# Kernel tuning notes

Hardware: AMD Instinct MI355X
Metric: run time of the kernel (lower is better)

Reference implementation:

```python
import jax, jax.numpy as jnp
import numpy as np

D = 768
NH = 12
HD = D // NH
N_MLP = 3072
LN_EPS = 1e-6


def layer_norm(x, g, b, eps=LN_EPS):
    mu = jnp.mean(x, axis=-1, keepdims=True)
    var = jnp.mean(jnp.square(x - mu), axis=-1, keepdims=True)
    return (x - mu) * jax.lax.rsqrt(var + eps) * g + b


def setup_inputs() -> dict:
    key = jax.random.key(0)
    ks = jax.random.split(key, 6)
    x = jax.random.normal(ks[0], (2, 4096, D), dtype=jnp.float32)
    # torch Linear weights are (out, in); init std=0.02, zero bias
    W_qkv = 0.02 * jax.random.normal(ks[1], (3 * D, D), dtype=jnp.float32)
    b_qkv = jnp.zeros((3 * D,), dtype=jnp.float32)
    W_proj = 0.02 * jax.random.normal(ks[2], (D, D), dtype=jnp.float32)
    b_proj = jnp.zeros((D,), dtype=jnp.float32)
    W1 = 0.02 * jax.random.normal(ks[3], (N_MLP, D), dtype=jnp.float32)
    b1 = jnp.zeros((N_MLP,), dtype=jnp.float32)
    W2 = 0.02 * jax.random.normal(ks[4], (D, N_MLP), dtype=jnp.float32)
    b2 = jnp.zeros((D,), dtype=jnp.float32)
    g1 = jnp.ones((D,), dtype=jnp.float32)
    beta1 = jnp.zeros((D,), dtype=jnp.float32)
    g2 = jnp.ones((D,), dtype=jnp.float32)
    beta2 = jnp.zeros((D,), dtype=jnp.float32)
    return dict(x=x, W_qkv=W_qkv, b_qkv=b_qkv, W_proj=W_proj, b_proj=b_proj,
                W1=W1, b1=b1, W2=W2, b2=b2,
                g1=g1, beta1=beta1, g2=g2, beta2=beta2)


def reference(x, W_qkv, b_qkv, W_proj, b_proj, W1, b1, W2, b2, g1, beta1, g2, beta2):
    B, T, d = x.shape
    scale = HD ** (-0.5)
    # --- attention branch (pre-norm) ---
    h = layer_norm(x, g1, beta1)
    qkv = h @ W_qkv.T + b_qkv                      # [B,T,3d]
    qkv = qkv.reshape(B, T, 3, NH, HD)
    q, k, v = qkv[:, :, 0], qkv[:, :, 1], qkv[:, :, 2]  # [B,T,NH,HD]
    logits = jnp.einsum('bthc,bshc->bhts', q, k) * scale
    attn = jax.nn.softmax(logits, axis=-1)
    out = jnp.einsum('bhts,bshc->bthc', attn, v).reshape(B, T, d)
    out = out @ W_proj.T + b_proj
    x = x + out
    # --- MLP branch (pre-norm) ---
    h = layer_norm(x, g2, beta2)
    h = jax.nn.gelu(h @ W1.T + b1, approximate=False)
    h = h @ W2.T + b2
    return x + h
```

## Files before the change

kernel.cpp:

```cpp
#include <hip/hip_runtime.h>
#include <cmath>

typedef __attribute__((ext_vector_type(4))) float f32x4;
typedef __attribute__((ext_vector_type(16))) float f32x16;
typedef __attribute__((ext_vector_type(8))) __bf16 bf16x8;
typedef __attribute__((ext_vector_type(8))) unsigned short u16x8;
typedef __attribute__((ext_vector_type(4))) unsigned short u16x4;
typedef __attribute__((ext_vector_type(2))) unsigned int u32x2;
typedef __attribute__((ext_vector_type(4))) unsigned int u32x4;

#define DEV __device__ __forceinline__

DEV unsigned short f2b(float v) {
  __bf16 b = (__bf16)v;
  return __builtin_bit_cast(unsigned short, b);
}

DEV unsigned int cvtpk(float lo, float hi) {
  unsigned int r;
  asm("v_cvt_pk_bf16_f32 %0, %1, %2" : "=v"(r) : "v"(lo), "v"(hi));
  return r;
}

DEV float exp2a(float x) {
  float r;
  asm("v_exp_f32 %0, %1" : "=v"(r) : "v"(x));
  return r;
}

DEV void swap32(unsigned int& x, unsigned int& y) {
  asm("v_permlane32_swap_b32 %0, %1" : "+v"(x), "+v"(y));
}

DEV u32x2 tr_b16(const unsigned short* p) {
  u32x2 r;
  asm volatile("ds_read_b64_tr_b16 %0, %1"
               : "=v"(r)
               : "v"((unsigned int)(unsigned long long)p)
               : "memory");
  return r;
}

DEV void gll16(const void* g, const void* l) {
  __builtin_amdgcn_global_load_lds(
      (const __attribute__((address_space(1))) unsigned int*)(unsigned long long)g,
      (__attribute__((address_space(3))) unsigned int*)(unsigned int)(unsigned long long)l,
      16, 0, 0);
}

__global__ void k_cvt_bf16(const float* __restrict__ src,
                           unsigned short* __restrict__ dst, int n4) {
  int i = blockIdx.x * blockDim.x + threadIdx.x;
  if (i >= n4) return;
  float4 v = ((const float4*)src)[i];
  u16x4 o = {f2b(v.x), f2b(v.y), f2b(v.z), f2b(v.w)};
  *(u16x4*)(dst + (size_t)i * 4) = o;
}

__global__ void k_ln(const float* __restrict__ x, const float* __restrict__ g,
                     const float* __restrict__ be, unsigned short* __restrict__ out) {
  int row = blockIdx.x;
  int l = threadIdx.x;
  const float* xr = x + (size_t)row * 768;
  float4 v[3];
  float s = 0.f, sq = 0.f;
#pragma unroll
  for (int j = 0; j < 3; ++j) {
    v[j] = ((const float4*)xr)[l + 64 * j];
    s += v[j].x + v[j].y + v[j].z + v[j].w;
    sq += v[j].x * v[j].x + v[j].y * v[j].y + v[j].z * v[j].z + v[j].w * v[j].w;
  }
#pragma unroll
  for (int m = 1; m < 64; m <<= 1) {
    s += __shfl_xor(s, m);
    sq += __shfl_xor(sq, m);
  }
  float mu = s * (1.f / 768.f);
  float var = sq * (1.f / 768.f) - mu * mu;
  float rs = rsqrtf(var + 1e-6f);
  unsigned short* orow = out + (size_t)row * 768;
#pragma unroll
  for (int j = 0; j < 3; ++j) {
    int c4 = l + 64 * j;
    float4 gv = ((const float4*)g)[c4];
    float4 bv = ((const float4*)be)[c4];
    u16x4 o = {f2b((v[j].x - mu) * rs * gv.x + bv.x),
               f2b((v[j].y - mu) * rs * gv.y + bv.y),
               f2b((v[j].z - mu) * rs * gv.z + bv.z),
               f2b((v[j].w - mu) * rs * gv.w + bv.w)};
    *(u16x4*)(orow + c4 * 4) = o;
  }
}

template <int MODE>
__global__ __launch_bounds__(256) void k_gemm(
    const unsigned short* __restrict__ A, const unsigned short* __restrict__ Bw,
    const float* __restrict__ bias, const float* __restrict__ res,
    void* __restrict__ outp, int N, int K) {
  __shared__ unsigned short As[128 * 32];
  __shared__ unsigned short Bs[128 * 32];
  const int tid = threadIdx.x;
  const int w = tid >> 6, l = tid & 63;
  const int wr = w >> 1, wc = w & 1;
  const int lr = l & 15, lg = l >> 4;
  const int nwg = gridDim.x * gridDim.y;
  const int bid = blockIdx.y * gridDim.x + blockIdx.x;
  const int swz = (bid & 7) * (nwg >> 3) + (bid >> 3);
  const int bx = swz % gridDim.x, by = swz / gridDim.x;
  const int brow = by * 128, bcol = bx * 128;
  f32x4 acc[4][4] = {};
  for (int kt = 0; kt < K; kt += 32) {
    __syncthreads();
#pragma unroll
    for (int i = 0; i < 2; ++i) {
      int c = i * 256 + tid;
      gll16(A + (size_t)(brow + (c >> 2)) * K + kt + (c & 3) * 8,
            (const char*)As + (i * 256 + (w << 6)) * 16);
      gll16(Bw + (size_t)(bcol + (c >> 2)) * K + kt + (c & 3) * 8,
            (const char*)Bs + (i * 256 + (w << 6)) * 16);
    }
    asm volatile("s_waitcnt vmcnt(0)" ::: "memory");
    __syncthreads();
    bf16x8 af[4], bfr[4];
#pragma unroll
    for (int m = 0; m < 4; ++m)
      af[m] = *(const bf16x8*)&As[(wr * 64 + m * 16 + lr) * 32 + lg * 8];
#pragma unroll
    for (int n = 0; n < 4; ++n)
      bfr[n] = *(const bf16x8*)&Bs[(wc * 64 + n * 16 + lr) * 32 + lg * 8];
#pragma unroll
    for (int m = 0; m < 4; ++m)
#pragma unroll
      for (int n = 0; n < 4; ++n)
        acc[m][n] = __builtin_amdgcn_mfma_f32_16x16x32_bf16(af[m], bfr[n], acc[m][n], 0, 0, 0);
  }
#pragma unroll
  for (int n = 0; n < 4; ++n) {
    int col = bcol + wc * 64 + n * 16 + lr;
    float bv = bias[col];
#pragma unroll
    for (int m = 0; m < 4; ++m) {
      int row0 = brow + wr * 64 + m * 16 + lg * 4;
#pragma unroll
      for (int r = 0; r < 4; ++r) {
        size_t idx = (size_t)(row0 + r) * N + col;
        float v = acc[m][n][r] + bv;
        if (MODE == 0) {
          ((unsigned short*)outp)[idx] = f2b(v);
        } else if (MODE == 1) {
          ((float*)outp)[idx] = v + res[idx];
        } else if (MODE == 2) {
          ((unsigned short*)outp)[idx] = f2b(0.5f * v * (1.f + erff(v * 0.70710678f)));
        } else {
          ((float*)outp)[idx] = v + res[idx];
        }
      }
    }
  }
}

__global__ __launch_bounds__(256, 3) void k_attn(const unsigned short* __restrict__ qkv,
                                                 unsigned short* __restrict__ out) {
  __shared__ unsigned short Ks[2][64 * 64];
  __shared__ unsigned short Vs[2][4 * 64 * 16];
  const int tid = threadIdx.x;
  const int w = tid >> 6, l = tid & 63;
  const int lq = l & 31, hi = l >> 5;
  const int p = blockIdx.x;
  const int bid = (p & 7) * 96 + (p >> 3);
  const int bh = bid >> 5, qt = bid & 31;
  const int b = bh / 12, h = bh % 12;
  const size_t base = (size_t)b * 4096 * 2304;
  const int qbase = qt * 128 + w * 32;

  const float SC = 0.18033688f;
  bf16x8 qb[4];
#pragma unroll
  for (int s = 0; s < 4; ++s) {
    u16x8 raw = *(const u16x8*)(qkv + base + (size_t)(qbase + lq) * 2304 + h * 64 +
                                s * 16 + hi * 8);
    u32x4 pk;
#pragma unroll
    for (int d = 0; d < 4; ++d) {
      float f0 = __builtin_bit_cast(float, (unsigned int)raw[2 * d] << 16) * SC;
      float f1 = __builtin_bit_cast(float, (unsigned int)raw[2 * d + 1] << 16) * SC;
      pk[d] = cvtpk(f0, f1);
    }
    qb[s] = __builtin_bit_cast(bf16x8, pk);
  }

  f32x16 O[2] = {};
  float mrun = -1e30f, lrun = 0.f;

  u16x8 kc[2], vc[2];
#pragma unroll
  for (int i = 0; i < 2; ++i) {
    int c = i * 256 + tid;
    const unsigned short* src = qkv + base + (size_t)(c >> 3) * 2304 + h * 64 + (c & 7) * 8;
    kc[i] = *(const u16x8*)(src + 768);
    vc[i] = *(const u16x8*)(src + 1536);
  }

  int it = 0;
  for (int kv = 0; kv < 4096; kv += 64, it ^= 1) {
#pragma unroll
    for (int i = 0; i < 2; ++i) {
      int c = i * 256 + tid;
      int key = c >> 3, a = c & 7;
      *(u16x8*)&Ks[it][key * 64 + ((a * 8) ^ ((key & 7) << 3))] = kc[i];
      *(u16x8*)&Vs[it][(a >> 1) * 1024 + key * 16 + (a & 1) * 8] = vc[i];
    }
    __syncthreads();

    {
      int kvn = (kv + 64) & 4095;
#pragma unroll
      for (int i = 0; i < 2; ++i) {
        int c = i * 256 + tid;
        const unsigned short* src =
            qkv + base + (size_t)(kvn + (c >> 3)) * 2304 + h * 64 + (c & 7) * 8;
        kc[i] = *(const u16x8*)(src + 768);
        vc[i] = *(const u16x8*)(src + 1536);
      }
    }

    f32x16 st[2] = {{0}, {0}};
    __builtin_amdgcn_s_setprio(1);
#pragma unroll
    for (int kt = 0; kt < 2; ++kt) {
      int key = kt * 32 + lq;
#pragma unroll
      for (int s = 0; s < 4; ++s) {
        bf16x8 ka =
            *(const bf16x8*)&Ks[it][key * 64 + ((s * 16 + hi * 8) ^ ((key & 7) << 3))];
        st[kt] = __builtin_amdgcn_mfma_f32_32x32x16_bf16(ka, qb[s], st[kt], 0, 0, 0);
      }
    }
    __builtin_amdgcn_s_setprio(0);

    float pmax = st[0][0];
#pragma unroll
    for (int kt = 0; kt < 2; ++kt)
#pragma unroll
      for (int r = (kt == 0 ? 1 : 0); r < 16; ++r) pmax = fmaxf(pmax, st[kt][r]);
    pmax = fmaxf(pmax, __shfl_xor(pmax, 32));
    if (!__all(pmax - mrun <= 11.0f)) {
      float mnew = fmaxf(mrun, pmax);
      float al = exp2a(mrun - mnew);
      lrun *= al;
#pragma unroll
      for (int hb = 0; hb < 2; ++hb)
#pragma unroll
        for (int r = 0; r < 16; ++r) O[hb][r] *= al;
      mrun = mnew;
    }
    float s0 = 0.f;
#pragma unroll
    for (int kt = 0; kt < 2; ++kt)
#pragma unroll
      for (int r = 0; r < 16; ++r) {
        float pv = exp2a(st[kt][r] - mrun);
        st[kt][r] = pv;
        s0 += pv;
      }
    lrun += s0 + __shfl_xor(s0, 32);

    u32x4 pf[4];
#pragma unroll
    for (int kt = 0; kt < 2; ++kt)
#pragma unroll
      for (int h2 = 0; h2 < 2; ++h2) {
        int r0 = h2 * 8;
        unsigned int a0 = cvtpk(st[kt][r0 + 0], st[kt][r0 + 1]);
        unsigned int a1 = cvtpk(st[kt][r0 + 2], st[kt][r0 + 3]);
        unsigned int b0 = cvtpk(st[kt][r0 + 4], st[kt][r0 + 5]);
        unsigned int b1 = cvtpk(st[kt][r0 + 6], st[kt][r0 + 7]);
        swap32(a0, b0);
        swap32(a1, b1);
        pf[kt * 2 + h2] = u32x4{a0, a1, b0, b1};
      }

#pragma unroll
    for (int hb = 0; hb < 2; ++hb) {
      u32x2 vt[4][2];
      const unsigned short* vbase = &Vs[it][(hb * 2 + (lq >> 4)) * 1024 + (lq & 15)];
#pragma unroll
      for (int s = 0; s < 4; ++s)
#pragma unroll
        for (int t = 0; t < 2; ++t)
          vt[s][t] = tr_b16(vbase + ((s * 16 + hi * 8 + t * 4) << 4));
      asm volatile("s_waitcnt lgkmcnt(0)" ::: "memory");
      __builtin_amdgcn_sched_barrier(0);
      __builtin_amdgcn_s_setprio(1);
#pragma unroll
      for (int s = 0; s < 4; ++s) {
        u32x4 vv = {vt[s][0].x, vt[s][0].y, vt[s][1].x, vt[s][1].y};
        O[hb] = __builtin_amdgcn_mfma_f32_32x32x16_bf16(
            __builtin_bit_cast(bf16x8, vv), __builtin_bit_cast(bf16x8, pf[s]), O[hb], 0, 0, 0);
      }
      __builtin_amdgcn_s_setprio(0);
    }
  }

  float rl = 1.f / lrun;
  unsigned short* orow = out + (size_t)(b * 4096 + qbase + lq) * 768 + h * 64;
#pragma unroll
  for (int hb = 0; hb < 2; ++hb)
#pragma unroll
    for (int g = 0; g < 4; ++g) {
      unsigned int d0 = cvtpk(O[hb][4 * g + 0] * rl, O[hb][4 * g + 1] * rl);
      unsigned int d1 = cvtpk(O[hb][4 * g + 2] * rl, O[hb][4 * g + 3] * rl);
      *(u32x2*)(orow + hb * 32 + 8 * g + 4 * hi) = u32x2{d0, d1};
    }
}

extern "C" void kernel_launch(void* const* d_in, const int* in_sizes, int n_in,
                              void* d_out, int out_size, void* d_ws, size_t ws_size,
                              hipStream_t stream) {
  const float* x = (const float*)d_in[0];
  const float* Wqkv = (const float*)d_in[1];
  const float* bqkv = (const float*)d_in[2];
  const float* Wproj = (const float*)d_in[3];
  const float* bproj = (const float*)d_in[4];
  const float* W1 = (const float*)d_in[5];
  const float* b1 = (const float*)d_in[6];
  const float* W2 = (const float*)d_in[7];
  const float* b2 = (const float*)d_in[8];
  const float* g1 = (const float*)d_in[9];
  const float* be1 = (const float*)d_in[10];
  const float* g2 = (const float*)d_in[11];
  const float* be2 = (const float*)d_in[12];

  char* ws = (char*)d_ws;
  unsigned short* wqkv = (unsigned short*)(ws + 0);
  unsigned short* wproj = (unsigned short*)(ws + 3538944);
  unsigned short* ww1 = (unsigned short*)(ws + 4718592);
  unsigned short* ww2 = (unsigned short*)(ws + 9437184);
  unsigned short* h1 = (unsigned short*)(ws + 14155776);
  unsigned short* qkvb = (unsigned short*)(ws + 26738688);
  unsigned short* attno = (unsigned short*)(ws + 64487424);
  float* x1 = (float*)(ws + 77070336);
  unsigned short* h2 = (unsigned short*)(ws + 102236160);
  unsigned short* m1 = (unsigned short*)(ws + 114819072);

  k_cvt_bf16<<<1728, 256, 0, stream>>>(Wqkv, wqkv, 442368);
  k_cvt_bf16<<<576, 256, 0, stream>>>(Wproj, wproj, 147456);
  k_cvt_bf16<<<2304, 256, 0, stream>>>(W1, ww1, 589824);
  k_cvt_bf16<<<2304, 256, 0, stream>>>(W2, ww2, 589824);

  k_ln<<<8192, 64, 0, stream>>>(x, g1, be1, h1);
  k_gemm<0><<<dim3(18, 64), 256, 0, stream>>>(h1, wqkv, bqkv, nullptr, qkvb, 2304, 768);
  k_attn<<<768, 256, 0, stream>>>(qkvb, attno);
  k_gemm<1><<<dim3(6, 64), 256, 0, stream>>>(attno, wproj, bproj, x, x1, 768, 768);
  k_ln<<<8192, 64, 0, stream>>>(x1, g2, be2, h2);
  k_gemm<2><<<dim3(24, 64), 256, 0, stream>>>(h2, ww1, b1, nullptr, m1, 3072, 768);
  k_gemm<3><<<dim3(6, 64), 256, 0, stream>>>(m1, ww2, b2, x1, (float*)d_out, 768, 3072);
}
```

Baseline: 382.0 us.

## Load attention K/V tiles via direct global-to-LDS and shrink narrow GEMM tiles

The attention kernel now prefetches K and V tiles into the other LDS buffer with direct global-to-LDS loads, replacing the register round-trip and explicit LDS stores. The source addresses are arranged so the existing swizzle and V layout still hold. Separately, the GEMM gains a BM template parameter, and the two N=768 GEMMs use 64-row tiles to double block count and fill more CUs. Risks include a full vmcnt wait each iteration and lower per-block reuse in the smaller-tile GEMMs.

```diff
diff --git a/kernel.cpp b/kernel.cpp
--- a/kernel.cpp
+++ b/kernel.cpp
@@ -92,13 +92,15 @@
   }
 }
 
-template <int MODE>
+template <int MODE, int BM>
 __global__ __launch_bounds__(256) void k_gemm(
     const unsigned short* __restrict__ A, const unsigned short* __restrict__ Bw,
     const float* __restrict__ bias, const float* __restrict__ res,
     void* __restrict__ outp, int N, int K) {
-  __shared__ unsigned short As[128 * 32];
+  __shared__ unsigned short As[BM * 32];
   __shared__ unsigned short Bs[128 * 32];
+  constexpr int MR = BM / 32;
+  constexpr int AI = BM / 64;
   const int tid = threadIdx.x;
   const int w = tid >> 6, l = tid & 63;
   const int wr = w >> 1, wc = w & 1;
@@ -107,29 +109,33 @@
   const int bid = blockIdx.y * gridDim.x + blockIdx.x;
   const int swz = (bid & 7) * (nwg >> 3) + (bid >> 3);
   const int bx = swz % gridDim.x, by = swz / gridDim.x;
-  const int brow = by * 128, bcol = bx * 128;
-  f32x4 acc[4][4] = {};
+  const int brow = by * BM, bcol = bx * 128;
+  f32x4 acc[MR][4] = {};
   for (int kt = 0; kt < K; kt += 32) {
     __syncthreads();
 #pragma unroll
-    for (int i = 0; i < 2; ++i) {
+    for (int i = 0; i < AI; ++i) {
       int c = i * 256 + tid;
       gll16(A + (size_t)(brow + (c >> 2)) * K + kt + (c & 3) * 8,
             (const char*)As + (i * 256 + (w << 6)) * 16);
+    }
+#pragma unroll
+    for (int i = 0; i < 2; ++i) {
+      int c = i * 256 + tid;
       gll16(Bw + (size_t)(bcol + (c >> 2)) * K + kt + (c & 3) * 8,
             (const char*)Bs + (i * 256 + (w << 6)) * 16);
     }
     asm volatile("s_waitcnt vmcnt(0)" ::: "memory");
     __syncthreads();
-    bf16x8 af[4], bfr[4];
-#pragma unroll
-    for (int m = 0; m < 4; ++m)
-      af[m] = *(const bf16x8*)&As[(wr * 64 + m * 16 + lr) * 32 + lg * 8];
+    bf16x8 af[MR], bfr[4];
+#pragma unroll
+    for (int m = 0; m < MR; ++m)
+      af[m] = *(const bf16x8*)&As[(wr * (BM / 2) + m * 16 + lr) * 32 + lg * 8];
 #pragma unroll
     for (int n = 0; n < 4; ++n)
       bfr[n] = *(const bf16x8*)&Bs[(wc * 64 + n * 16 + lr) * 32 + lg * 8];
 #pragma unroll
-    for (int m = 0; m < 4; ++m)
+    for (int m = 0; m < MR; ++m)
 #pragma unroll
       for (int n = 0; n < 4; ++n)
         acc[m][n] = __builtin_amdgcn_mfma_f32_16x16x32_bf16(af[m], bfr[n], acc[m][n], 0, 0, 0);
@@ -139,8 +145,8 @@
     int col = bcol + wc * 64 + n * 16 + lr;
     float bv = bias[col];
 #pragma unroll
-    for (int m = 0; m < 4; ++m) {
-      int row0 = brow + wr * 64 + m * 16 + lg * 4;
+    for (int m = 0; m < MR; ++m) {
+      int row0 = brow + wr * (BM / 2) + m * 16 + lg * 4;
 #pragma unroll
       for (int r = 0; r < 4; ++r) {
         size_t idx = (size_t)(row0 + r) * N + col;
@@ -189,39 +195,39 @@
     qb[s] = __builtin_bit_cast(bf16x8, pk);
   }
 
+  const unsigned short* pK = qkv + base + (size_t)(16 * w + (l >> 3)) * 2304 + 768 +
+                             h * 64 + (((l & 7) ^ ((l >> 3) & 7)) << 3);
+  const unsigned short* pV =
+      qkv + base + (size_t)(l >> 1) * 2304 + 1536 + h * 64 + w * 16 + ((l & 1) << 3);
+  const size_t STEP = (size_t)64 * 2304;
+
+  {
+    const char* dK = (const char*)&Ks[0][0] + w * 2048;
+    const char* dV = (const char*)&Vs[0][0] + w * 2048;
+    gll16(pK, dK);
+    gll16(pK + 8 * 2304, dK + 1024);
+    gll16(pV, dV);
+    gll16(pV + 32 * 2304, dV + 1024);
+    pK += STEP;
+    pV += STEP;
+  }
+
   f32x16 O[2] = {};
   float mrun = -1e30f, lrun = 0.f;
 
-  u16x8 kc[2], vc[2];
-#pragma unroll
-  for (int i = 0; i < 2; ++i) {
-    int c = i * 256 + tid;
-    const unsigned short* src = qkv + base + (size_t)(c >> 3) * 2304 + h * 64 + (c & 7) * 8;
-    kc[i] = *(const u16x8*)(src + 768);
-    vc[i] = *(const u16x8*)(src + 1536);
-  }
-
   int it = 0;
-  for (int kv = 0; kv < 4096; kv += 64, it ^= 1) {
-#pragma unroll
-    for (int i = 0; i < 2; ++i) {
-      int c = i * 256 + tid;
-      int key = c >> 3, a = c & 7;
-      *(u16x8*)&Ks[it][key * 64 + ((a * 8) ^ ((key & 7) << 3))] = kc[i];
-      *(u16x8*)&Vs[it][(a >> 1) * 1024 + key * 16 + (a & 1) * 8] = vc[i];
-    }
+  for (int t = 0; t < 64; ++t, it ^= 1) {
+    asm volatile("s_waitcnt vmcnt(0)" ::: "memory");
     __syncthreads();
-
-    {
-      int kvn = (kv + 64) & 4095;
-#pragma unroll
-      for (int i = 0; i < 2; ++i) {
-        int c = i * 256 + tid;
-        const unsigned short* src =
-            qkv + base + (size_t)(kvn + (c >> 3)) * 2304 + h * 64 + (c & 7) * 8;
-        kc[i] = *(const u16x8*)(src + 768);
-        vc[i] = *(const u16x8*)(src + 1536);
-      }
+    if (t < 63) {
+      const char* dK = (const char*)&Ks[it ^ 1][0] + w * 2048;
+      const char* dV = (const char*)&Vs[it ^ 1][0] + w * 2048;
+      gll16(pK, dK);
+      gll16(pK + 8 * 2304, dK + 1024);
+      gll16(pV, dV);
+      gll16(pV + 32 * 2304, dV + 1024);
+      pK += STEP;
+      pV += STEP;
     }
 
     f32x16 st[2] = {{0}, {0}};
@@ -287,8 +293,8 @@
 #pragma unroll
       for (int s = 0; s < 4; ++s)
 #pragma unroll
-        for (int t = 0; t < 2; ++t)
-          vt[s][t] = tr_b16(vbase + ((s * 16 + hi * 8 + t * 4) << 4));
+        for (int t2 = 0; t2 < 2; ++t2)
+          vt[s][t2] = tr_b16(vbase + ((s * 16 + hi * 8 + t2 * 4) << 4));
       asm volatile("s_waitcnt lgkmcnt(0)" ::: "memory");
       __builtin_amdgcn_sched_barrier(0);
       __builtin_amdgcn_s_setprio(1);
@@ -349,10 +355,10 @@
   k_cvt_bf16<<<2304, 256, 0, stream>>>(W2, ww2, 589824);
 
   k_ln<<<8192, 64, 0, stream>>>(x, g1, be1, h1);
-  k_gemm<0><<<dim3(18, 64), 256, 0, stream>>>(h1, wqkv, bqkv, nullptr, qkvb, 2304, 768);
+  k_gemm<0, 128><<<dim3(18, 64), 256, 0, stream>>>(h1, wqkv, bqkv, nullptr, qkvb, 2304, 768);
   k_attn<<<768, 256, 0, stream>>>(qkvb, attno);
-  k_gemm<1><<<dim3(6, 64), 256, 0, stream>>>(attno, wproj, bproj, x, x1, 768, 768);
+  k_gemm<1, 64><<<dim3(6, 128), 256, 0, stream>>>(attno, wproj, bproj, x, x1, 768, 768);
   k_ln<<<8192, 64, 0, stream>>>(x1, g2, be2, h2);
-  k_gemm<2><<<dim3(24, 64), 256, 0, stream>>>(h2, ww1, b1, nullptr, m1, 3072, 768);
-  k_gemm<3><<<dim3(6, 64), 256, 0, stream>>>(m1, ww2, b2, x1, (float*)d_out, 768, 3072);
-}
+  k_gemm<2, 128><<<dim3(24, 64), 256, 0, stream>>>(h2, ww1, b1, nullptr, m1, 3072, 768);
+  k_gemm<3, 64><<<dim3(6, 128), 256, 0, stream>>>(m1, ww2, b2, x1, (float*)d_out, 768, 3072);
+}
```

Result: faster. 374.4 us (-2.0%).
